# Optimization experiments

Measured on AMD Instinct MI355X. Metric: run time of the kernel, lower is better.

The kernel has to match this reference:

```python
import jax, jax.numpy as jnp
import numpy as np

B, NW, LW = 128, 64, 32
TD, PD = 108, 19
F = PD + TD + 1   # feat_dim = 128
M = 128           # model_dim


def _linear_params(key, din, dout):
    kw, _ = jax.random.split(key)
    W = jax.random.normal(kw, (din, dout), jnp.float32) * 0.02
    b = jnp.zeros((dout,), jnp.float32)
    return W, b


def setup_inputs() -> dict:
    key = jax.random.key(0)
    ks = jax.random.split(key, 12)
    time_features = jax.random.normal(ks[0], (B, NW, LW, TD), jnp.float32)
    position_pos_features = jax.random.normal(ks[1], (B, NW, LW, PD), jnp.float32)
    position_neg_features = jax.random.normal(ks[2], (B, NW, LW, PD), jnp.float32)
    weight = jax.random.uniform(ks[3], (B, NW, LW), jnp.float32)
    # sign in {-1, +1} (0 would zero the step; walks are signed edges)
    sign = (2 * jax.random.randint(ks[4], (B, NW, LW), 0, 2) - 1).astype(jnp.int32)
    Wq, bq = _linear_params(ks[5], F, F)
    Wk, bk = _linear_params(ks[6], F, F)
    Wv, bv = _linear_params(ks[7], F, F)
    Wl, bl = _linear_params(ks[8], F, M)
    Wqp, bqp = _linear_params(ks[9], M, M)
    Wkp, bkp = _linear_params(ks[10], M, M)
    Wvp, bvp = _linear_params(ks[11], M, M)
    return dict(time_features=time_features,
                position_pos_features=position_pos_features,
                position_neg_features=position_neg_features,
                weight=weight, sign=sign,
                Wq=Wq, bq=bq, Wk=Wk, bk=bk, Wv=Wv, bv=bv,
                Wl=Wl, bl=bl,
                Wqp=Wqp, bqp=bqp, Wkp=Wkp, bkp=bkp, Wvp=Wvp, bvp=bvp)


def _self_attn_sum(x, Wq, bq, Wk, bk, Wv, bv):
    # x: [..., L, D]; manual scaled-dot attention, scale = sqrt(input_size)
    d = x.shape[-1]
    q = x @ Wq + bq
    k = x @ Wk + bk
    v = x @ Wv + bv
    scores = jnp.einsum('...ld,...md->...lm', q, k) / jnp.sqrt(jnp.float32(d))
    w = jax.nn.softmax(scores, axis=-1)
    av = jnp.einsum('...lm,...md->...ld', w, v)
    return av.sum(axis=-2)  # sum over query positions


def reference(time_features, position_pos_features, position_neg_features,
              weight, sign,
              Wq, bq, Wk, bk, Wv, bv, Wl, bl,
              Wqp, bqp, Wkp, bkp, Wvp, bvp):
    # concat_features (note arg swap in forward_one_node): [pos_feat, time_feat, weight]
    cp = jnp.concatenate([position_pos_features, time_features, weight[..., None]], axis=-1)
    cn = jnp.concatenate([position_neg_features, time_features, weight[..., None]], axis=-1)
    pm = (sign > 0)[..., None]
    nm = (sign < 0)[..., None]
    zero = jnp.zeros((), cp.dtype)
    positive = jnp.where(pm, cp, zero) + jnp.where(nm, cn, zero)  # [B,NW,LW,F]
    negative = jnp.where(pm, cn, zero) + jnp.where(nm, cp, zero)
    # per-walk self-attention over len_walk, summed -> [B,NW,F]
    pos_emb = _self_attn_sum(positive, Wq, bq, Wk, bk, Wv, bv)
    neg_emb = _self_attn_sum(negative, Wq, bq, Wk, bk, Wv, bv)
    # set_node_embedding_act linear (no nonlinearity in source)
    pos_emb = pos_emb @ Wl + bl  # [B,NW,M]
    neg_emb = neg_emb @ Wl + bl
    # path attention over n_walk, summed -> [B,M]
    pos = _self_attn_sum(pos_emb, Wqp, bqp, Wkp, bkp, Wvp, bvp)
    neg = _self_attn_sum(neg_emb, Wqp, bqp, Wkp, bkp, Wvp, bvp)
    return (pos, neg)
```

## Files before the change

kernel.cpp:

```cpp
#include <hip/hip_runtime.h>
#include <hip/hip_bf16.h>

typedef __hip_bfloat16 bf16;
typedef unsigned short u16;
typedef unsigned int   u32;
typedef __attribute__((ext_vector_type(8))) short short8;
typedef __attribute__((ext_vector_type(4))) float f32x4;
typedef __attribute__((ext_vector_type(4))) unsigned int u32x4;

#define SCALE 0.08838834764831845f
#define MFMA  __builtin_amdgcn_mfma_f32_16x16x32_bf16

__device__ __forceinline__ float u2f(u16 x) { return __uint_as_float(((u32)x) << 16); }
__device__ __forceinline__ u16   f2u(float f) {
    __hip_bfloat16 h = __float2bfloat16(f);
    return *reinterpret_cast<u16*>(&h);
}
__device__ __forceinline__ float lo16(u32 w){ return __uint_as_float(w << 16); }
__device__ __forceinline__ float hi16(u32 w){ return __uint_as_float(w & 0xffff0000u); }
__device__ __forceinline__ int swz(int row, int col){ return (row << 7) | (col ^ ((row & 7) << 3)); }

__global__ void prep_aq(const float* __restrict__ Wq,  const float* __restrict__ Wk,
                        const float* __restrict__ bq,
                        const float* __restrict__ Wqp, const float* __restrict__ Wkp,
                        const float* __restrict__ bqp,
                        u16* __restrict__ frag, float* __restrict__ vv) {
    const int b = blockIdx.x;
    const int p = b / 33, sub = b % 33;
    const float* WA = p ? Wqp : Wq;
    const float* WB = p ? Wkp : Wk;
    const float* bA = p ? bqp : bq;
    if (sub < 32) {
        const int nt = sub >> 2, kc = sub & 3;
        u16* dst = frag + p * 16384 + sub * 512;
        for (int e = threadIdx.x; e < 512; e += 256) {
            const int lane = e >> 3, j = e & 7;
            const int k = kc * 32 + ((lane >> 4) << 3) + j;
            const int n = nt * 16 + (lane & 15);
            float a = 0.f;
            for (int cc = 0; cc < 128; cc += 4) {
                const float4 wa = *(const float4*)(WA + k * 128 + cc);
                const float4 wb = *(const float4*)(WB + n * 128 + cc);
                a += wa.x * wb.x + wa.y * wb.y + wa.z * wb.z + wa.w * wb.w;
            }
            dst[e] = f2u(a * SCALE);
        }
    } else {
        for (int d = threadIdx.x; d < 128; d += 256) {
            float a = 0.f;
            for (int cc = 0; cc < 128; cc++) a += WB[d * 128 + cc] * bA[cc];
            vv[p * 128 + d] = a;
        }
    }
}

__global__ void prep_wvl(const float* __restrict__ Wv, const float* __restrict__ bv,
                         const float* __restrict__ Wl, const float* __restrict__ bl,
                         u16* __restrict__ wvlT, float* __restrict__ bvl) {
    const int d = threadIdx.x;
    const int e = blockIdx.x;
    if (e < 128) {
        float a = 0.f;
        for (int cc = 0; cc < 128; cc++) a += Wv[e * 128 + cc] * Wl[cc * 128 + d];
        wvlT[(d >> 1) * 256 + e * 2 + (d & 1)] = f2u(a);
    } else {
        float a = bl[d];
        for (int cc = 0; cc < 128; cc++) a += 32.f * bv[cc] * Wl[cc * 128 + d];
        bvl[d] = a;
    }
}

__global__ __launch_bounds__(256) void rwa_walk_wave(
    const float* __restrict__ timef, const float* __restrict__ ppf,
    const float* __restrict__ pnf,  const float* __restrict__ wgt,
    const int*  __restrict__ sgn,
    const u16* __restrict__ fragQ,
    const float* __restrict__ vk,
    const u16* __restrict__ wvlT,
    const float* __restrict__ bvl,
    u16* __restrict__ emb)
{
    __shared__ __align__(16) u16 XS[4][4096];
    __shared__ __align__(16) u16 TS[4][4096];
    const int t  = threadIdx.x;
    const int wv = t >> 6, l = t & 63;
    const int wid  = blockIdx.x * 4 + wv;
    const int walk = wid >> 1, side = wid & 1;
    const int c = l & 15, g = l >> 4;
    u16* const xw = &XS[wv][0];
    u16* const tw = &TS[wv][0];

    const int row = l & 31, h = l >> 5;
    const int tok = walk * 32 + row;
    const float* tfp = timef + tok * 108;
    float v[64];
    if (h == 0) {
        const float* pb = ((sgn[tok] > 0) == (side == 0)) ? (ppf + tok * 19) : (pnf + tok * 19);
        #pragma unroll
        for (int i = 0; i < 19; i++) v[i] = pb[i];
        #pragma unroll
        for (int i = 0; i < 11; i++) {
            const float4 q = *(const float4*)(tfp + 4 * i);
            v[19 + 4*i] = q.x; v[20 + 4*i] = q.y; v[21 + 4*i] = q.z; v[22 + 4*i] = q.w;
        }
        v[63] = tfp[44];
    } else {
        v[0] = tfp[45]; v[1] = tfp[46]; v[2] = tfp[47];
        #pragma unroll
        for (int i = 0; i < 15; i++) {
            const float4 q = *(const float4*)(tfp + 48 + 4 * i);
            v[3 + 4*i] = q.x; v[4 + 4*i] = q.y; v[5 + 4*i] = q.z; v[6 + 4*i] = q.w;
        }
        v[63] = wgt[tok];
    }
    float ra = 0.f;
    {
        const float* vkh = vk + h * 64;
        #pragma unroll
        for (int i = 0; i < 16; i++) {
            const float4 k4 = *(const float4*)(vkh + 4 * i);
            ra += v[4*i] * k4.x + v[4*i+1] * k4.y + v[4*i+2] * k4.z + v[4*i+3] * k4.w;
        }
    }
    #pragma unroll
    for (int ch = 0; ch < 8; ch++) {
        short8 pk;
        #pragma unroll
        for (int j = 0; j < 8; j++) pk[j] = (short)f2u(v[ch * 8 + j]);
        *(short8*)&xw[swz(row, h * 64 + ch * 8)] = pk;
    }
    ra += __shfl_xor(ra, 32);
    ra *= SCALE;
    __syncthreads();

    short8 af[2][4];
    #pragma unroll
    for (int it = 0; it < 2; it++)
        #pragma unroll
        for (int kc = 0; kc < 4; kc++)
            af[it][kc] = *(const short8*)&xw[swz(it * 16 + c, kc * 32 + g * 8)];
    #pragma unroll
    for (int nt = 0; nt < 8; nt++) {
        f32x4 a0 = {0.f, 0.f, 0.f, 0.f}, a1 = {0.f, 0.f, 0.f, 0.f};
        #pragma unroll
        for (int kc = 0; kc < 4; kc++) {
            const short8 bf = *(const short8*)(fragQ + ((nt * 4 + kc) * 64 + l) * 8);
            a0 = MFMA(af[0][kc], bf, a0, 0, 0, 0);
            a1 = MFMA(af[1][kc], bf, a1, 0, 0, 0);
        }
        #pragma unroll
        for (int r = 0; r < 4; r++) {
            tw[swz(g * 4 + r,      nt * 16 + c)] = f2u(a0[r]);
            tw[swz(16 + g * 4 + r, nt * 16 + c)] = f2u(a1[r]);
        }
    }
    __syncthreads();

    f32x4 sa[2][2];
    #pragma unroll
    for (int it = 0; it < 2; it++) {
        short8 tg[4];
        #pragma unroll
        for (int kc = 0; kc < 4; kc++)
            tg[kc] = *(const short8*)&tw[swz(it * 16 + c, kc * 32 + g * 8)];
        #pragma unroll
        for (int jt = 0; jt < 2; jt++) {
            f32x4 acc = {0.f, 0.f, 0.f, 0.f};
            #pragma unroll
            for (int kc = 0; kc < 4; kc++)
                acc = MFMA(tg[kc], af[jt][kc], acc, 0, 0, 0);
            sa[it][jt] = acc;
        }
    }
    const float ra0 = __shfl(ra, c);
    const float ra1 = __shfl(ra, 16 + c);
    float cs0 = 0.f, cs1 = 0.f;
    #pragma unroll
    for (int it = 0; it < 2; it++)
    #pragma unroll
    for (int r = 0; r < 4; r++) {
        const float s0v = sa[it][0][r] + ra0;
        const float s1v = sa[it][1][r] + ra1;
        float m0 = fmaxf(s0v, s1v);
        m0 = fmaxf(m0, __shfl_xor(m0, 1));
        m0 = fmaxf(m0, __shfl_xor(m0, 2));
        m0 = fmaxf(m0, __shfl_xor(m0, 4));
        m0 = fmaxf(m0, __shfl_xor(m0, 8));
        const float p0 = __expf(s0v - m0);
        const float p1 = __expf(s1v - m0);
        float sm = p0 + p1;
        sm += __shfl_xor(sm, 1); sm += __shfl_xor(sm, 2);
        sm += __shfl_xor(sm, 4); sm += __shfl_xor(sm, 8);
        const float inv = 1.f / sm;
        cs0 += p0 * inv; cs1 += p1 * inv;
    }
    cs0 += __shfl_xor(cs0, 16); cs0 += __shfl_xor(cs0, 32);
    cs1 += __shfl_xor(cs1, 16); cs1 += __shfl_xor(cs1, 32);

    float y0 = 0.f, y1v = 0.f;
    #pragma unroll
    for (int j = 0; j < 16; j++) {
        const float cj = __shfl(cs0, j);
        const u32 xv = *(const u32*)&xw[swz(j, 2 * l)];
        y0 += cj * lo16(xv); y1v += cj * hi16(xv);
    }
    #pragma unroll
    for (int j = 0; j < 16; j++) {
        const float cj = __shfl(cs1, j);
        const u32 xv = *(const u32*)&xw[swz(16 + j, 2 * l)];
        y0 += cj * lo16(xv); y1v += cj * hi16(xv);
    }

    const float2 bb = *(const float2*)&bvl[2 * l];
    float e0 = bb.x, e1 = bb.y;
    const u32* wrow = (const u32*)wvlT + l * 128;
    #pragma unroll
    for (int eq = 0; eq < 32; eq++) {
        const u32x4 w4 = *(const u32x4*)(wrow + 4 * eq);
        #pragma unroll
        for (int s = 0; s < 4; s++) {
            const int e = 4 * eq + s;
            const float ye = __shfl((e & 1) ? y1v : y0, e >> 1);
            e0 += ye * lo16(w4[s]); e1 += ye * hi16(w4[s]);
        }
    }
    const u32 pk = (u32)f2u(e0) | ((u32)f2u(e1) << 16);
    ((u32*)emb)[(side * 8192 + walk) * 64 + l] = pk;
}

__global__ __launch_bounds__(64) void rwa_path_wave(
    const u16* __restrict__ embg, const u16* __restrict__ fragP,
    const float* __restrict__ vp, const float* __restrict__ Wvp,
    const float* __restrict__ bvp, float* __restrict__ out)
{
    __shared__ __align__(16) u16 ES[8192];
    __shared__ __align__(16) u16 TS[8192];
    const int l = threadIdx.x;
    const int sb = blockIdx.x;
    const int c = l & 15, g = l >> 4;

    const u16* src = embg + (size_t)sb * 8192 + l * 128;
    float ra = 0.f;
    #pragma unroll
    for (int i = 0; i < 16; i++) {
        const short8 ev = *(const short8*)(src + 8 * i);
        const float4 p0 = *(const float4*)(vp + 8 * i);
        const float4 p1 = *(const float4*)(vp + 8 * i + 4);
        ra += u2f((u16)ev[0]) * p0.x + u2f((u16)ev[1]) * p0.y
            + u2f((u16)ev[2]) * p0.z + u2f((u16)ev[3]) * p0.w;
        ra += u2f((u16)ev[4]) * p1.x + u2f((u16)ev[5]) * p1.y
            + u2f((u16)ev[6]) * p1.z + u2f((u16)ev[7]) * p1.w;
        *(short8*)&ES[swz(l, 8 * i)] = ev;
    }
    ra *= SCALE;
    __syncthreads();

    #pragma unroll
    for (int it = 0; it < 4; it++) {
        short8 afr[4];
        #pragma unroll
        for (int kc = 0; kc < 4; kc++)
            afr[kc] = *(const short8*)&ES[swz(it * 16 + c, kc * 32 + g * 8)];
        #pragma unroll
        for (int nt = 0; nt < 8; nt++) {
            f32x4 acc = {0.f, 0.f, 0.f, 0.f};
            #pragma unroll
            for (int kc = 0; kc < 4; kc++) {
                const short8 bf = *(const short8*)(fragP + ((nt * 4 + kc) * 64 + l) * 8);
                acc = MFMA(afr[kc], bf, acc, 0, 0, 0);
            }
            #pragma unroll
            for (int r = 0; r < 4; r++)
                TS[swz(it * 16 + g * 4 + r, nt * 16 + c)] = f2u(acc[r]);
        }
    }
    __syncthreads();

    short8 be[4][4];
    #pragma unroll
    for (int jt = 0; jt < 4; jt++)
        #pragma unroll
        for (int kc = 0; kc < 4; kc++)
            be[jt][kc] = *(const short8*)&ES[swz(jt * 16 + c, kc * 32 + g * 8)];
    f32x4 sa[4][4];
    #pragma unroll
    for (int it = 0; it < 4; it++) {
        short8 tg[4];
        #pragma unroll
        for (int kc = 0; kc < 4; kc++)
            tg[kc] = *(const short8*)&TS[swz(it * 16 + c, kc * 32 + g * 8)];
        #pragma unroll
        for (int jt = 0; jt < 4; jt++) {
            f32x4 acc = {0.f, 0.f, 0.f, 0.f};
            #pragma unroll
            for (int kc = 0; kc < 4; kc++)
                acc = MFMA(tg[kc], be[jt][kc], acc, 0, 0, 0);
            sa[it][jt] = acc;
        }
    }
    float raj[4];
    #pragma unroll
    for (int jt = 0; jt < 4; jt++) raj[jt] = __shfl(ra, jt * 16 + c);
    float cs[4] = {0.f, 0.f, 0.f, 0.f};
    #pragma unroll
    for (int it = 0; it < 4; it++)
    #pragma unroll
    for (int r = 0; r < 4; r++) {
        float pv[4];
        #pragma unroll
        for (int jt = 0; jt < 4; jt++) pv[jt] = sa[it][jt][r] + raj[jt];
        float m0 = fmaxf(fmaxf(pv[0], pv[1]), fmaxf(pv[2], pv[3]));
        m0 = fmaxf(m0, __shfl_xor(m0, 1));
        m0 = fmaxf(m0, __shfl_xor(m0, 2));
        m0 = fmaxf(m0, __shfl_xor(m0, 4));
        m0 = fmaxf(m0, __shfl_xor(m0, 8));
        float sm = 0.f;
        #pragma unroll
        for (int jt = 0; jt < 4; jt++) { pv[jt] = __expf(pv[jt] - m0); sm += pv[jt]; }
        sm += __shfl_xor(sm, 1); sm += __shfl_xor(sm, 2);
        sm += __shfl_xor(sm, 4); sm += __shfl_xor(sm, 8);
        const float inv = 1.f / sm;
        #pragma unroll
        for (int jt = 0; jt < 4; jt++) cs[jt] += pv[jt] * inv;
    }
    #pragma unroll
    for (int jt = 0; jt < 4; jt++) {
        cs[jt] += __shfl_xor(cs[jt], 16);
        cs[jt] += __shfl_xor(cs[jt], 32);
    }

    float y0 = 0.f, y1v = 0.f;
    #pragma unroll
    for (int j = 0; j < 64; j++) {
        const float cj = __shfl(cs[j >> 4], j & 15);
        const u32 xv = *(const u32*)&ES[swz(j, 2 * l)];
        y0 += cj * lo16(xv); y1v += cj * hi16(xv);
    }

    const float2 bb = *(const float2*)&bvp[2 * l];
    float o0 = 64.f * bb.x, o1 = 64.f * bb.y;
    #pragma unroll
    for (int e = 0; e < 128; e++) {
        const float ye = __shfl((e & 1) ? y1v : y0, e >> 1);
        const float2 w2 = *(const float2*)&Wvp[e * 128 + 2 * l];
        o0 += ye * w2.x; o1 += ye * w2.y;
    }
    *(float2*)&out[sb * 128 + 2 * l] = make_float2(o0, o1);
}

__global__ __launch_bounds__(256) void rwa_fused_fb(
    const float* timef, const float* ppf, const float* pnf, const float* wgt,
    const int* __restrict__ sgn,
    const float* Wq, const float* bq, const float* Wk, const float* bk,
    const float* Wv, const float* bv, const float* Wl, const float* bl,
    const float* Wqp, const float* bqp, const float* Wkp, const float* bkp,
    const float* Wvp, const float* bvp, float* out)
{
    extern __shared__ __align__(16) char S[];
    char* const U = S;
    float (* const sc)[33]     = (float(*)[33])(S + 41088);
    u16   (* const embs)[128]  = (u16  (*)[128])(S + 45312);
    float* const csumA         = (float*)(S + 61696);
    float* const y1            = (float*)(S + 61824);
    float* const e1            = (float*)(S + 62336);
    u16   (* const xs)[128]   = (u16  (*)[128])U;
    float (* const qs)[128]   = (float(*)[128])(U + 8192);
    float (* const ks)[129]   = (float(*)[129])(U + 8192 + 16384);
    float (* const k2s)[129]  = (float(*)[129])U;
    float (* const qrow)[128] = (float(*)[128])(U + 33024);
    float (* const csum2)[64] = (float(*)[64])(U + 35072);

    const int t    = threadIdx.x;
    const int side = blockIdx.x >> 7;
    const int b    = blockIdx.x & 127;
    const int wv_  = t >> 6;
    const int lane = t & 63;

    for (int w = 0; w < 64; ++w) {
        const int tokb = (b * 64 + w) * 32;
        for (int o = t; o < 32 * 128; o += 256) {
            const int l = o >> 7, f = o & 127;
            const int tok = tokb + l;
            float v;
            if (f < 19) {
                const bool takeP = (sgn[tok] > 0) == (side == 0);
                v = takeP ? ppf[tok * 19 + f] : pnf[tok * 19 + f];
            } else if (f < 127) v = timef[tok * 108 + (f - 19)];
            else v = wgt[tok];
            xs[l][f] = f2u(v);
        }
        __syncthreads();
        {
            const int d = t & 127, l0 = t >> 7;
            float aq[16], ak[16];
            const float bqv = bq[d], bkv = bk[d];
            #pragma unroll
            for (int i = 0; i < 16; i++) { aq[i] = bqv; ak[i] = bkv; }
            for (int e = 0; e < 128; e += 4) {
                float xv[16][4];
                #pragma unroll
                for (int i = 0; i < 16; i++) {
                    const ushort4 u = *(const ushort4*)&xs[l0 + 2 * i][e];
                    xv[i][0] = u2f(u.x); xv[i][1] = u2f(u.y);
                    xv[i][2] = u2f(u.z); xv[i][3] = u2f(u.w);
                }
                #pragma unroll
                for (int r = 0; r < 4; r++) {
                    const float wq = Wq[(e + r) * 128 + d];
                    const float wk = Wk[(e + r) * 128 + d];
                    #pragma unroll
                    for (int i = 0; i < 16; i++) {
                        aq[i] += xv[i][r] * wq; ak[i] += xv[i][r] * wk;
                    }
                }
            }
            #pragma unroll
            for (int i = 0; i < 16; i++) { const int l = l0 + 2 * i; qs[l][d] = aq[i]; ks[l][d] = ak[i]; }
        }
        __syncthreads();
        for (int o = t; o < 1024; o += 256) {
            const int i = o >> 5, j = o & 31;
            float a0 = 0, a1 = 0, a2 = 0, a3 = 0;
            for (int e = 0; e < 128; e += 4) {
                const float4 q4 = *(const float4*)&qs[i][e];
                a0 += q4.x * ks[j][e];     a1 += q4.y * ks[j][e + 1];
                a2 += q4.z * ks[j][e + 2]; a3 += q4.w * ks[j][e + 3];
            }
            sc[i][j] = (a0 + a1 + a2 + a3) * SCALE;
        }
        __syncthreads();
        if (t < 32) {
            float m = -1e30f;
            for (int j = 0; j < 32; j++) m = fmaxf(m, sc[t][j]);
            float s = 0.f;
            for (int j = 0; j < 32; j++) { const float e0 = __expf(sc[t][j] - m); sc[t][j] = e0; s += e0; }
            const float inv = 1.f / s;
            for (int j = 0; j < 32; j++) sc[t][j] *= inv;
        }
        __syncthreads();
        if (t < 32) { float s = 0.f; for (int i = 0; i < 32; i++) s += sc[i][t]; csumA[t] = s; }
        __syncthreads();
        if (t < 128) { float a = 0.f; for (int j = 0; j < 32; j++) a += csumA[j] * u2f(xs[j][t]); y1[t] = a; }
        __syncthreads();
        if (t < 128) {
            float a = 32.f * bv[t];
            for (int e = 0; e < 128; e++) a += y1[e] * Wv[e * 128 + t];
            e1[t] = a;
        }
        __syncthreads();
        if (t < 128) {
            float a = bl[t];
            for (int f = 0; f < 128; f++) a += e1[f] * Wl[f * 128 + t];
            embs[w][t] = f2u(a);
        }
        __syncthreads();
    }
    {
        const int d = t & 127, j0 = t >> 7;
        float ak2[32];
        const float bkv = bkp[d];
        #pragma unroll
        for (int i = 0; i < 32; i++) ak2[i] = bkv;
        for (int e = 0; e < 128; e++) {
            const float wk = Wkp[e * 128 + d];
            #pragma unroll
            for (int i = 0; i < 32; i++) ak2[i] += u2f(embs[j0 + 2 * i][e]) * wk;
        }
        #pragma unroll
        for (int i = 0; i < 32; i++) k2s[j0 + 2 * i][d] = ak2[i];
    }
    csum2[wv_][lane] = 0.f;
    __syncthreads();
    for (int i0 = 0; i0 < 64; i0 += 4) {
        const int r = i0 + wv_;
        {
            float a0 = bqp[lane], a1 = bqp[lane + 64];
            for (int e = 0; e < 128; e++) {
                const float xv = u2f(embs[r][e]);
                a0 += xv * Wqp[e * 128 + lane];
                a1 += xv * Wqp[e * 128 + lane + 64];
            }
            qrow[wv_][lane] = a0; qrow[wv_][lane + 64] = a1;
        }
        {
            const int j = lane;
            float s = 0.f;
            for (int e = 0; e < 128; e += 4) {
                const float4 q4 = *(const float4*)&qrow[wv_][e];
                s += q4.x * k2s[j][e] + q4.y * k2s[j][e + 1] + q4.z * k2s[j][e + 2] + q4.w * k2s[j][e + 3];
            }
            s *= SCALE;
            float m = s;
            #pragma unroll
            for (int off = 32; off; off >>= 1) m = fmaxf(m, __shfl_xor(m, off));
            const float e0 = __expf(s - m);
            float sum = e0;
            #pragma unroll
            for (int off = 32; off; off >>= 1) sum += __shfl_xor(sum, off);
            csum2[wv_][j] += e0 / sum;
        }
        __syncthreads();
    }
    if (t < 64) csum2[0][t] = csum2[0][t] + csum2[1][t] + csum2[2][t] + csum2[3][t];
    __syncthreads();
    if (t < 128) { float a = 0.f; for (int j = 0; j < 64; j++) a += csum2[0][j] * u2f(embs[j][t]); y1[t] = a; }
    __syncthreads();
    if (t < 128) {
        float a = 64.f * bvp[t];
        for (int e = 0; e < 128; e++) a += y1[e] * Wvp[e * 128 + t];
        out[blockIdx.x * 128 + t] = a;
    }
}

extern "C" void kernel_launch(void* const* d_in, const int* in_sizes, int n_in,
                              void* d_out, int out_size, void* d_ws, size_t ws_size,
                              hipStream_t stream) {
    const float* timef = (const float*)d_in[0];
    const float* ppf   = (const float*)d_in[1];
    const float* pnf   = (const float*)d_in[2];
    const float* wgt   = (const float*)d_in[3];
    const int*   sgn   = (const int*)  d_in[4];
    const float* Wq  = (const float*)d_in[5];  const float* bq  = (const float*)d_in[6];
    const float* Wk  = (const float*)d_in[7];  const float* bk  = (const float*)d_in[8];
    const float* Wv  = (const float*)d_in[9];  const float* bv  = (const float*)d_in[10];
    const float* Wl  = (const float*)d_in[11]; const float* bl  = (const float*)d_in[12];
    const float* Wqp = (const float*)d_in[13]; const float* bqp = (const float*)d_in[14];
    const float* Wkp = (const float*)d_in[15]; const float* bkp = (const float*)d_in[16];
    const float* Wvp = (const float*)d_in[17]; const float* bvp = (const float*)d_in[18];
    float* out = (float*)d_out;
    (void)in_sizes; (void)n_in; (void)out_size;

    const size_t need = 99840 + (size_t)2 * 8192 * 128 * sizeof(u16);
    if (ws_size >= need) {
        u16*   frag = (u16*)d_ws;
        float* vv   = (float*)((char*)d_ws + 65536);
        u16*   wvlT = (u16*)((char*)d_ws + 66560);
        float* bvl  = (float*)((char*)d_ws + 99328);
        u16*   emb  = (u16*)((char*)d_ws + 99840);
        hipLaunchKernelGGL(prep_aq,  dim3(66),  dim3(256), 0, stream,
                           Wq, Wk, bq, Wqp, Wkp, bqp, frag, vv);
        hipLaunchKernelGGL(prep_wvl, dim3(129), dim3(128), 0, stream, Wv, bv, Wl, bl, wvlT, bvl);
        hipLaunchKernelGGL(rwa_walk_wave, dim3(4096), dim3(256), 0, stream,
                           timef, ppf, pnf, wgt, sgn, frag, vv, wvlT, bvl, emb);
        hipLaunchKernelGGL(rwa_path_wave, dim3(256), dim3(64), 0, stream,
                           emb, frag + 16384, vv + 128, Wvp, bvp, out);
    } else {
        hipLaunchKernelGGL(rwa_fused_fb, dim3(256), dim3(256), 62848, stream,
                           timef, ppf, pnf, wgt, sgn, Wq, bq, Wk, bk, Wv, bv, Wl, bl,
                           Wqp, bqp, Wkp, bkp, Wvp, bvp, out);
    }
}
```

Before: 407.2 us.

## Halve walk-kernel LDS, drop block barriers, and split path kernel across four waves

The walk kernel reuses a single per-wave LDS tile for both X and the Q-projected T instead of a separate TS buffer. It also drops the block-level __syncthreads, since each wave owns its tile, and restores X from registers after the score step. The final Wvl projection now reads y through LDS as float4 instead of 128 shuffles, and launch bounds ask for 5 blocks per CU. The path kernel moves from one wave to four waves per block, splitting rows and reductions across waves with LDS partial sums. This adds parallelism for a grid of only 256 blocks, at the cost of extra barriers and reliance on wave-synchronous LDS ordering.

```diff
diff --git a/kernel.cpp b/kernel.cpp
--- a/kernel.cpp
+++ b/kernel.cpp
@@ -70,7 +70,7 @@
     }
 }
 
-__global__ __launch_bounds__(256) void rwa_walk_wave(
+__global__ __launch_bounds__(256, 5) void rwa_walk_wave(
     const float* __restrict__ timef, const float* __restrict__ ppf,
     const float* __restrict__ pnf,  const float* __restrict__ wgt,
     const int*  __restrict__ sgn,
@@ -81,14 +81,12 @@
     u16* __restrict__ emb)
 {
     __shared__ __align__(16) u16 XS[4][4096];
-    __shared__ __align__(16) u16 TS[4][4096];
     const int t  = threadIdx.x;
     const int wv = t >> 6, l = t & 63;
     const int wid  = blockIdx.x * 4 + wv;
     const int walk = wid >> 1, side = wid & 1;
     const int c = l & 15, g = l >> 4;
     u16* const xw = &XS[wv][0];
-    u16* const tw = &TS[wv][0];
 
     const int row = l & 31, h = l >> 5;
     const int tok = walk * 32 + row;
@@ -131,7 +129,6 @@
     }
     ra += __shfl_xor(ra, 32);
     ra *= SCALE;
-    __syncthreads();
 
     short8 af[2][4];
     #pragma unroll
@@ -139,6 +136,7 @@
         #pragma unroll
         for (int kc = 0; kc < 4; kc++)
             af[it][kc] = *(const short8*)&xw[swz(it * 16 + c, kc * 32 + g * 8)];
+
     #pragma unroll
     for (int nt = 0; nt < 8; nt++) {
         f32x4 a0 = {0.f, 0.f, 0.f, 0.f}, a1 = {0.f, 0.f, 0.f, 0.f};
@@ -150,11 +148,10 @@
         }
         #pragma unroll
         for (int r = 0; r < 4; r++) {
-            tw[swz(g * 4 + r,      nt * 16 + c)] = f2u(a0[r]);
-            tw[swz(16 + g * 4 + r, nt * 16 + c)] = f2u(a1[r]);
-        }
-    }
-    __syncthreads();
+            xw[swz(g * 4 + r,      nt * 16 + c)] = f2u(a0[r]);
+            xw[swz(16 + g * 4 + r, nt * 16 + c)] = f2u(a1[r]);
+        }
+    }
 
     f32x4 sa[2][2];
     #pragma unroll
@@ -162,7 +159,7 @@
         short8 tg[4];
         #pragma unroll
         for (int kc = 0; kc < 4; kc++)
-            tg[kc] = *(const short8*)&tw[swz(it * 16 + c, kc * 32 + g * 8)];
+            tg[kc] = *(const short8*)&xw[swz(it * 16 + c, kc * 32 + g * 8)];
         #pragma unroll
         for (int jt = 0; jt < 2; jt++) {
             f32x4 acc = {0.f, 0.f, 0.f, 0.f};
@@ -197,6 +194,12 @@
     cs0 += __shfl_xor(cs0, 16); cs0 += __shfl_xor(cs0, 32);
     cs1 += __shfl_xor(cs1, 16); cs1 += __shfl_xor(cs1, 32);
 
+    #pragma unroll
+    for (int it = 0; it < 2; it++)
+        #pragma unroll
+        for (int kc = 0; kc < 4; kc++)
+            *(short8*)&xw[swz(it * 16 + c, kc * 32 + g * 8)] = af[it][kc];
+
     float y0 = 0.f, y1v = 0.f;
     #pragma unroll
     for (int j = 0; j < 16; j++) {
@@ -211,52 +214,61 @@
         y0 += cj * lo16(xv); y1v += cj * hi16(xv);
     }
 
+    float* const yb = (float*)xw;
+    *(float2*)&yb[2 * l] = make_float2(y0, y1v);
+
     const float2 bb = *(const float2*)&bvl[2 * l];
     float e0 = bb.x, e1 = bb.y;
     const u32* wrow = (const u32*)wvlT + l * 128;
+    const float4* yf = (const float4*)yb;
     #pragma unroll
     for (int eq = 0; eq < 32; eq++) {
         const u32x4 w4 = *(const u32x4*)(wrow + 4 * eq);
-        #pragma unroll
-        for (int s = 0; s < 4; s++) {
-            const int e = 4 * eq + s;
-            const float ye = __shfl((e & 1) ? y1v : y0, e >> 1);
-            e0 += ye * lo16(w4[s]); e1 += ye * hi16(w4[s]);
-        }
+        const float4 y4 = yf[eq];
+        e0 += y4.x * lo16(w4[0]) + y4.y * lo16(w4[1]) + y4.z * lo16(w4[2]) + y4.w * lo16(w4[3]);
+        e1 += y4.x * hi16(w4[0]) + y4.y * hi16(w4[1]) + y4.z * hi16(w4[2]) + y4.w * hi16(w4[3]);
     }
     const u32 pk = (u32)f2u(e0) | ((u32)f2u(e1) << 16);
     ((u32*)emb)[(side * 8192 + walk) * 64 + l] = pk;
 }
 
-__global__ __launch_bounds__(64) void rwa_path_wave(
+__global__ __launch_bounds__(256) void rwa_path_wave(
     const u16* __restrict__ embg, const u16* __restrict__ fragP,
     const float* __restrict__ vp, const float* __restrict__ Wvp,
     const float* __restrict__ bvp, float* __restrict__ out)
 {
     __shared__ __align__(16) u16 ES[8192];
     __shared__ __align__(16) u16 TS[8192];
-    const int l = threadIdx.x;
+    __shared__ float raS[64];
+    __shared__ float csP[4][64];
+    __shared__ float y2S[4][128];
+    __shared__ float y2F[128];
+    __shared__ float outS[4][128];
+    const int t  = threadIdx.x;
     const int sb = blockIdx.x;
+    const int wv = t >> 6, l = t & 63;
     const int c = l & 15, g = l >> 4;
 
-    const u16* src = embg + (size_t)sb * 8192 + l * 128;
-    float ra = 0.f;
-    #pragma unroll
-    for (int i = 0; i < 16; i++) {
-        const short8 ev = *(const short8*)(src + 8 * i);
-        const float4 p0 = *(const float4*)(vp + 8 * i);
-        const float4 p1 = *(const float4*)(vp + 8 * i + 4);
-        ra += u2f((u16)ev[0]) * p0.x + u2f((u16)ev[1]) * p0.y
-            + u2f((u16)ev[2]) * p0.z + u2f((u16)ev[3]) * p0.w;
-        ra += u2f((u16)ev[4]) * p1.x + u2f((u16)ev[5]) * p1.y
-            + u2f((u16)ev[6]) * p1.z + u2f((u16)ev[7]) * p1.w;
-        *(short8*)&ES[swz(l, 8 * i)] = ev;
-    }
-    ra *= SCALE;
-    __syncthreads();
-
-    #pragma unroll
-    for (int it = 0; it < 4; it++) {
+    {
+        const int row = t >> 2, q = t & 3;
+        const u16* src = embg + (size_t)sb * 8192 + row * 128 + q * 32;
+        const float* vq = vp + q * 32;
+        float p = 0.f;
+        #pragma unroll
+        for (int i = 0; i < 4; i++) {
+            const short8 ev = *(const short8*)(src + 8 * i);
+            #pragma unroll
+            for (int j = 0; j < 8; j++) p += u2f((u16)ev[j]) * vq[8 * i + j];
+            *(short8*)&ES[swz(row, q * 32 + 8 * i)] = ev;
+        }
+        p += __shfl_xor(p, 1);
+        p += __shfl_xor(p, 2);
+        if (q == 0) raS[row] = p * SCALE;
+    }
+    __syncthreads();
+
+    {
+        const int it = wv;
         short8 afr[4];
         #pragma unroll
         for (int kc = 0; kc < 4; kc++)
@@ -276,76 +288,85 @@
     }
     __syncthreads();
 
-    short8 be[4][4];
-    #pragma unroll
-    for (int jt = 0; jt < 4; jt++)
-        #pragma unroll
-        for (int kc = 0; kc < 4; kc++)
-            be[jt][kc] = *(const short8*)&ES[swz(jt * 16 + c, kc * 32 + g * 8)];
-    f32x4 sa[4][4];
-    #pragma unroll
-    for (int it = 0; it < 4; it++) {
+    {
+        const int it = wv;
         short8 tg[4];
         #pragma unroll
         for (int kc = 0; kc < 4; kc++)
             tg[kc] = *(const short8*)&TS[swz(it * 16 + c, kc * 32 + g * 8)];
+        f32x4 sa[4];
+        float raj[4];
         #pragma unroll
         for (int jt = 0; jt < 4; jt++) {
             f32x4 acc = {0.f, 0.f, 0.f, 0.f};
             #pragma unroll
-            for (int kc = 0; kc < 4; kc++)
-                acc = MFMA(tg[kc], be[jt][kc], acc, 0, 0, 0);
-            sa[it][jt] = acc;
-        }
-    }
-    float raj[4];
-    #pragma unroll
-    for (int jt = 0; jt < 4; jt++) raj[jt] = __shfl(ra, jt * 16 + c);
-    float cs[4] = {0.f, 0.f, 0.f, 0.f};
-    #pragma unroll
-    for (int it = 0; it < 4; it++)
-    #pragma unroll
-    for (int r = 0; r < 4; r++) {
-        float pv[4];
-        #pragma unroll
-        for (int jt = 0; jt < 4; jt++) pv[jt] = sa[it][jt][r] + raj[jt];
-        float m0 = fmaxf(fmaxf(pv[0], pv[1]), fmaxf(pv[2], pv[3]));
-        m0 = fmaxf(m0, __shfl_xor(m0, 1));
-        m0 = fmaxf(m0, __shfl_xor(m0, 2));
-        m0 = fmaxf(m0, __shfl_xor(m0, 4));
-        m0 = fmaxf(m0, __shfl_xor(m0, 8));
-        float sm = 0.f;
-        #pragma unroll
-        for (int jt = 0; jt < 4; jt++) { pv[jt] = __expf(pv[jt] - m0); sm += pv[jt]; }
-        sm += __shfl_xor(sm, 1); sm += __shfl_xor(sm, 2);
-        sm += __shfl_xor(sm, 4); sm += __shfl_xor(sm, 8);
-        const float inv = 1.f / sm;
-        #pragma unroll
-        for (int jt = 0; jt < 4; jt++) cs[jt] += pv[jt] * inv;
-    }
-    #pragma unroll
-    for (int jt = 0; jt < 4; jt++) {
-        cs[jt] += __shfl_xor(cs[jt], 16);
-        cs[jt] += __shfl_xor(cs[jt], 32);
-    }
-
-    float y0 = 0.f, y1v = 0.f;
-    #pragma unroll
-    for (int j = 0; j < 64; j++) {
-        const float cj = __shfl(cs[j >> 4], j & 15);
-        const u32 xv = *(const u32*)&ES[swz(j, 2 * l)];
-        y0 += cj * lo16(xv); y1v += cj * hi16(xv);
-    }
-
-    const float2 bb = *(const float2*)&bvp[2 * l];
-    float o0 = 64.f * bb.x, o1 = 64.f * bb.y;
-    #pragma unroll
-    for (int e = 0; e < 128; e++) {
-        const float ye = __shfl((e & 1) ? y1v : y0, e >> 1);
-        const float2 w2 = *(const float2*)&Wvp[e * 128 + 2 * l];
-        o0 += ye * w2.x; o1 += ye * w2.y;
-    }
-    *(float2*)&out[sb * 128 + 2 * l] = make_float2(o0, o1);
+            for (int kc = 0; kc < 4; kc++) {
+                const short8 be = *(const short8*)&ES[swz(jt * 16 + c, kc * 32 + g * 8)];
+                acc = MFMA(tg[kc], be, acc, 0, 0, 0);
+            }
+            sa[jt] = acc;
+            raj[jt] = raS[jt * 16 + c];
+        }
+        float cs[4] = {0.f, 0.f, 0.f, 0.f};
+        #pragma unroll
+        for (int r = 0; r < 4; r++) {
+            float p0 = sa[0][r] + raj[0], p1 = sa[1][r] + raj[1];
+            float p2 = sa[2][r] + raj[2], p3 = sa[3][r] + raj[3];
+            float m0 = fmaxf(fmaxf(p0, p1), fmaxf(p2, p3));
+            m0 = fmaxf(m0, __shfl_xor(m0, 1));
+            m0 = fmaxf(m0, __shfl_xor(m0, 2));
+            m0 = fmaxf(m0, __shfl_xor(m0, 4));
+            m0 = fmaxf(m0, __shfl_xor(m0, 8));
+            p0 = __expf(p0 - m0); p1 = __expf(p1 - m0);
+            p2 = __expf(p2 - m0); p3 = __expf(p3 - m0);
+            float sm = p0 + p1 + p2 + p3;
+            sm += __shfl_xor(sm, 1); sm += __shfl_xor(sm, 2);
+            sm += __shfl_xor(sm, 4); sm += __shfl_xor(sm, 8);
+            const float inv = 1.f / sm;
+            cs[0] += p0 * inv; cs[1] += p1 * inv; cs[2] += p2 * inv; cs[3] += p3 * inv;
+        }
+        #pragma unroll
+        for (int jt = 0; jt < 4; jt++) {
+            cs[jt] += __shfl_xor(cs[jt], 16);
+            cs[jt] += __shfl_xor(cs[jt], 32);
+        }
+        if (g == 0) {
+            #pragma unroll
+            for (int jt = 0; jt < 4; jt++) csP[wv][jt * 16 + c] = cs[jt];
+        }
+    }
+    __syncthreads();
+
+    {
+        float y0 = 0.f, y1v = 0.f;
+        #pragma unroll
+        for (int jj = 0; jj < 16; jj++) {
+            const int j = wv * 16 + jj;
+            const float cj = csP[0][j] + csP[1][j] + csP[2][j] + csP[3][j];
+            const u32 xv = *(const u32*)&ES[swz(j, 2 * l)];
+            y0 += cj * lo16(xv); y1v += cj * hi16(xv);
+        }
+        y2S[wv][2 * l] = y0; y2S[wv][2 * l + 1] = y1v;
+    }
+    __syncthreads();
+    if (t < 128) y2F[t] = y2S[0][t] + y2S[1][t] + y2S[2][t] + y2S[3][t];
+    __syncthreads();
+
+    {
+        float o0 = 0.f, o1 = 0.f;
+        const float2* w2p = (const float2*)Wvp;
+        #pragma unroll
+        for (int k = 0; k < 32; k++) {
+            const int e = wv * 32 + k;
+            const float ye = y2F[e];
+            const float2 w2 = w2p[e * 64 + l];
+            o0 += ye * w2.x; o1 += ye * w2.y;
+        }
+        outS[wv][2 * l] = o0; outS[wv][2 * l + 1] = o1;
+    }
+    __syncthreads();
+    if (t < 128)
+        out[sb * 128 + t] = 64.f * bvp[t] + outS[0][t] + outS[1][t] + outS[2][t] + outS[3][t];
 }
 
 __global__ __launch_bounds__(256) void rwa_fused_fb(
@@ -542,7 +563,7 @@
         hipLaunchKernelGGL(prep_wvl, dim3(129), dim3(128), 0, stream, Wv, bv, Wl, bl, wvlT, bvl);
         hipLaunchKernelGGL(rwa_walk_wave, dim3(4096), dim3(256), 0, stream,
                            timef, ppf, pnf, wgt, sgn, frag, vv, wvlT, bvl, emb);
-        hipLaunchKernelGGL(rwa_path_wave, dim3(256), dim3(64), 0, stream,
+        hipLaunchKernelGGL(rwa_path_wave, dim3(256), dim3(256), 0, stream,
                            emb, frag + 16384, vv + 128, Wvp, bvp, out);
     } else {
         hipLaunchKernelGGL(rwa_fused_fb, dim3(256), dim3(256), 62848, stream,
```

After: 521.7 us. 28.1% more time.
